# Optimization experiments

Measured on AMD Instinct MI355X. Metric: run time of the kernel, lower is better.

## Reference

```python
import jax, jax.numpy as jnp
import numpy as np

NUM_PATCHES_SIDE = 32
LOCAL_RADIUS = 3.0


def _build_non_local_mask():
    # coords of each patch on the grid, matching torch.meshgrid(indexing='ij')
    h = np.arange(NUM_PATCHES_SIDE)
    hh, ww = np.meshgrid(h, h, indexing='ij')
    coors = np.stack([hh, ww], axis=0).astype(np.float32)  # (2, H, W)
    coors = coors.reshape(2, -1).T                          # (n, 2)
    dist = np.linalg.norm(coors[:, None, :] - coors[None, :, :], axis=-1)
    return jnp.asarray(dist > LOCAL_RADIUS)                 # (n, n) bool


def setup_inputs() -> dict:
    key = jax.random.key(0)
    b, n, l, d = 8, NUM_PATCHES_SIDE * NUM_PATCHES_SIDE, 6, 512
    levels = jax.random.normal(key, (b, n, l, d), dtype=jnp.float32)
    non_local_mask = _build_non_local_mask()
    return {"levels": levels, "non_local_mask": non_local_mask}


def reference(levels, non_local_mask):
    b, n, l, d = levels.shape
    # F.normalize(levels, dim=-1): x / max(||x||, eps)
    norm = jnp.linalg.norm(levels, axis=-1, keepdims=True)
    k = levels / jnp.maximum(norm, 1e-12)
    # scores per level: (b, l, n, n)
    sim = jnp.einsum('bild,bjld->blij', levels, k) * (d ** -0.5)
    max_neg = -jnp.finfo(sim.dtype).max
    sim = jnp.where(non_local_mask[None, None, :, :], max_neg, sim)
    attn = jax.nn.softmax(sim, axis=-1)
    out = jnp.einsum('blij,bjld->bild', attn, levels)
    return out
```

## Files before the change

kernel.cpp:

```cpp
#include <hip/hip_runtime.h>
#include <math.h>

#define NPS 32
#define NN  (NPS*NPS)
#define LL  6
#define DD  512
#define ROWSPB (NN*LL)
#define BIAS 576

#define INV_SQRT_D 0.044194173824159216f
#define LOG2E      1.4426950408889634f
#define KLOG       (INV_SQRT_D * LOG2E)

__device__ __forceinline__ float half_sum32(float x) {
    int t;
    t = __builtin_amdgcn_update_dpp(0, __float_as_int(x), 0xB1, 0xF, 0xF, true);
    x += __int_as_float(t);
    t = __builtin_amdgcn_update_dpp(0, __float_as_int(x), 0x4E, 0xF, 0xF, true);
    x += __int_as_float(t);
    t = __builtin_amdgcn_update_dpp(0, __float_as_int(x), 0x141, 0xF, 0xF, true);
    x += __int_as_float(t);
    t = __builtin_amdgcn_update_dpp(0, __float_as_int(x), 0x140, 0xF, 0xF, true);
    x += __int_as_float(t);
    x += __int_as_float(__builtin_amdgcn_ds_swizzle(__float_as_int(x), 0x401F));
    return x;
}

__device__ __forceinline__ float wave_sum_bcast(float x) {
    x = half_sum32(x);
    x += __shfl_xor(x, 32, 64);
    return x;
}

__device__ __forceinline__ float dot16(const float4& a0, const float4& a1,
                                       const float4& a2, const float4& a3,
                                       const float4& b0, const float4& b1,
                                       const float4& b2, const float4& b3) {
    float d = a0.x * b0.x;
    d = fmaf(a0.y, b0.y, d); d = fmaf(a0.z, b0.z, d); d = fmaf(a0.w, b0.w, d);
    d = fmaf(a1.x, b1.x, d); d = fmaf(a1.y, b1.y, d); d = fmaf(a1.z, b1.z, d);
    d = fmaf(a1.w, b1.w, d);
    d = fmaf(a2.x, b2.x, d); d = fmaf(a2.y, b2.y, d); d = fmaf(a2.z, b2.z, d);
    d = fmaf(a2.w, b2.w, d);
    d = fmaf(a3.x, b3.x, d); d = fmaf(a3.y, b3.y, d); d = fmaf(a3.z, b3.z, d);
    d = fmaf(a3.w, b3.w, d);
    return d;
}

__global__ __launch_bounds__(256) void ca_norm2(const float* __restrict__ levels,
                                                float* __restrict__ cws,
                                                float* __restrict__ mws, int rows) {
    int tid  = threadIdx.x;
    int lane = tid & 63;
    int sl   = lane & 31;
    int grp  = lane >> 5;
    int w = ((int)blockIdx.x * 4 + (tid >> 6)) * 2 + grp;
    if (w >= rows) return;
    const float4* x4 = (const float4*)(levels + (unsigned)(w * DD));
    float4 a0 = x4[sl], a1 = x4[sl+32], a2 = x4[sl+64], a3 = x4[sl+96];
    float s2 = dot16(a0,a1,a2,a3, a0,a1,a2,a3);
    s2 = half_sum32(s2);
    if (sl == 0) {
        float r = __frsqrt_rn(s2);
        cws[w] = KLOG * r;
        mws[w] = KLOG * s2 * r;
    }
}

__global__ __launch_bounds__(256) void ca_fused4(const float* __restrict__ levels,
                                                 const float* __restrict__ cws,
                                                 const float* __restrict__ mws,
                                                 float* __restrict__ out, int rows) {
    constexpr int NIT = 18;
    constexpr int typ [NIT] = { 2, 2, 2, 2, 2, 2, 2, 2, 2, 2,  0, 0, 0, 0,  1, 1, 1, 1};
    constexpr int dhA_[NIT] = {-2,-2,-1,-1, 0, 0, 1, 1, 2, 2, -3,-2,-1, 0, -3,-2,-1, 0};
    constexpr int duA_[NIT] = {-1, 0,-1, 0,-2,-1,-1, 0,-1, 0,  0,-2,-2,-3,  1, 3, 3, 0};
    constexpr int dhB_[NIT] = {-2,-2,-1,-1, 0, 0, 1, 1, 2, 2,  0, 1, 2, 3,  0, 1, 2, 3};
    constexpr int duB_[NIT] = { 1, 2, 1, 2, 2, 3, 1, 2, 1, 2,  1,-2,-2, 0,  4, 3, 3, 1};

    unsigned bk    = blockIdx.x;
    unsigned chunk = gridDim.x >> 3;
    unsigned vb    = (bk & 7) * chunk + (bk >> 3);

    int tid  = threadIdx.x;
    int lane = tid & 63;
    int sl   = lane & 31;
    bool hi  = lane >= 32;

    int b  = (int)(vb / 768u);
    int r1 = (int)(vb - (unsigned)b * 768u);
    int pg = r1 / 6;
    int l  = r1 - pg * 6;
    int p0 = pg * 8 + ((tid >> 6) << 1);
    int w0 = __builtin_amdgcn_readfirstlane(b * ROWSPB + p0 * LL + l);
    if (w0 >= rows) return;
    int ph  = p0 >> 5;
    int pw0 = p0 & 31;

    const float4* x0 = (const float4*)(levels + (size_t)w0 * DD);
    const float4* x1 = x0 + (DD / 4) * LL;
    float4 a00 = x0[sl], a01 = x0[sl+32], a02 = x0[sl+64], a03 = x0[sl+96];
    float4 a10 = x1[sl], a11 = x1[sl+32], a12 = x1[sl+64], a13 = x1[sl+96];

    float m20 = mws[w0];
    float m21 = mws[w0 + LL];

    float  lsum0 = 0.0f, lsum1 = 0.0f;
    float4 c00 = make_float4(0,0,0,0), c01 = make_float4(0,0,0,0);
    float4 c02 = make_float4(0,0,0,0), c03 = make_float4(0,0,0,0);
    float4 c10 = make_float4(0,0,0,0), c11 = make_float4(0,0,0,0);
    float4 c12 = make_float4(0,0,0,0), c13 = make_float4(0,0,0,0);

    const char* lvb = (const char*)levels + ((long long)w0 - BIAS) * (DD * 4);
    const char* cwb = (const char*)cws    + ((long long)w0 - BIAS) * 4;

    #pragma unroll
    for (int t = 0; t < NIT; ++t) {
        const int dA = dhA_[t], uA = duA_[t];
        const int dB = dhB_[t], uB = duB_[t];
        bool vA = ((unsigned)(ph + dA) < (unsigned)NPS) &&
                  ((unsigned)(pw0 + uA) < (unsigned)NPS);
        bool vB = ((unsigned)(ph + dB) < (unsigned)NPS) &&
                  ((unsigned)(pw0 + uB) < (unsigned)NPS);
        int offA = ((vA ? (dA * NPS + uA) * LL : 0) + BIAS) * (DD * 4);
        int offB = ((vB ? (dB * NPS + uB) * LL : 0) + BIAS) * (DD * 4);
        int off  = hi ? offB : offA;
        const char* bp = lvb + off;
        float4 b0 = *(const float4*)(bp + sl * 16);
        float4 b1 = *(const float4*)(bp + sl * 16 + 512);
        float4 b2 = *(const float4*)(bp + sl * 16 + 1024);
        float4 b3 = *(const float4*)(bp + sl * 16 + 1536);
        float  cj = *(const float*)(cwb + (off >> 9));
        float  vm = (hi ? vB : vA) ? 1.0f : 0.0f;

        float d0 = 0.f, d1 = 0.f;
        if (typ[t] != 1) d0 = dot16(a00,a01,a02,a03, b0,b1,b2,b3);
        if (typ[t] != 0) d1 = dot16(a10,a11,a12,a13, b0,b1,b2,b3);
        if (typ[t] != 1) d0 = half_sum32(d0);
        if (typ[t] != 0) d1 = half_sum32(d1);

        if (typ[t] != 1) {
            float pr0 = vm * __builtin_amdgcn_exp2f(fmaf(d0, cj, -m20));
            lsum0 += pr0;
            c00.x = fmaf(pr0, b0.x, c00.x); c00.y = fmaf(pr0, b0.y, c00.y);
            c00.z = fmaf(pr0, b0.z, c00.z); c00.w = fmaf(pr0, b0.w, c00.w);
            c01.x = fmaf(pr0, b1.x, c01.x); c01.y = fmaf(pr0, b1.y, c01.y);
            c01.z = fmaf(pr0, b1.z, c01.z); c01.w = fmaf(pr0, b1.w, c01.w);
            c02.x = fmaf(pr0, b2.x, c02.x); c02.y = fmaf(pr0, b2.y, c02.y);
            c02.z = fmaf(pr0, b2.z, c02.z); c02.w = fmaf(pr0, b2.w, c02.w);
            c03.x = fmaf(pr0, b3.x, c03.x); c03.y = fmaf(pr0, b3.y, c03.y);
            c03.z = fmaf(pr0, b3.z, c03.z); c03.w = fmaf(pr0, b3.w, c03.w);
        }
        if (typ[t] != 0) {
            float pr1 = vm * __builtin_amdgcn_exp2f(fmaf(d1, cj, -m21));
            lsum1 += pr1;
            c10.x = fmaf(pr1, b0.x, c10.x); c10.y = fmaf(pr1, b0.y, c10.y);
            c10.z = fmaf(pr1, b0.z, c10.z); c10.w = fmaf(pr1, b0.w, c10.w);
            c11.x = fmaf(pr1, b1.x, c11.x); c11.y = fmaf(pr1, b1.y, c11.y);
            c11.z = fmaf(pr1, b1.z, c11.z); c11.w = fmaf(pr1, b1.w, c11.w);
            c12.x = fmaf(pr1, b2.x, c12.x); c12.y = fmaf(pr1, b2.y, c12.y);
            c12.z = fmaf(pr1, b2.z, c12.z); c12.w = fmaf(pr1, b2.w, c12.w);
            c13.x = fmaf(pr1, b3.x, c13.x); c13.y = fmaf(pr1, b3.y, c13.y);
            c13.z = fmaf(pr1, b3.z, c13.z); c13.w = fmaf(pr1, b3.w, c13.w);
        }
    }

    #define CMB(v) v += __shfl_xor(v, 32, 64)
    CMB(lsum0); CMB(lsum1);
    CMB(c00.x); CMB(c00.y); CMB(c00.z); CMB(c00.w);
    CMB(c01.x); CMB(c01.y); CMB(c01.z); CMB(c01.w);
    CMB(c02.x); CMB(c02.y); CMB(c02.z); CMB(c02.w);
    CMB(c03.x); CMB(c03.y); CMB(c03.z); CMB(c03.w);
    CMB(c10.x); CMB(c10.y); CMB(c10.z); CMB(c10.w);
    CMB(c11.x); CMB(c11.y); CMB(c11.z); CMB(c11.w);
    CMB(c12.x); CMB(c12.y); CMB(c12.z); CMB(c12.w);
    CMB(c13.x); CMB(c13.y); CMB(c13.z); CMB(c13.w);
    #undef CMB

    lsum0 += 1.0f; lsum1 += 1.0f;
    c00.x += a00.x; c00.y += a00.y; c00.z += a00.z; c00.w += a00.w;
    c01.x += a01.x; c01.y += a01.y; c01.z += a01.z; c01.w += a01.w;
    c02.x += a02.x; c02.y += a02.y; c02.z += a02.z; c02.w += a02.w;
    c03.x += a03.x; c03.y += a03.y; c03.z += a03.z; c03.w += a03.w;
    c10.x += a10.x; c10.y += a10.y; c10.z += a10.z; c10.w += a10.w;
    c11.x += a11.x; c11.y += a11.y; c11.z += a11.z; c11.w += a11.w;
    c12.x += a12.x; c12.y += a12.y; c12.z += a12.z; c12.w += a12.w;
    c13.x += a13.x; c13.y += a13.y; c13.z += a13.z; c13.w += a13.w;

    float  inv = 1.0f / (hi ? lsum1 : lsum0);
    float4 s0 = hi ? c10 : c00;
    float4 s1 = hi ? c11 : c01;
    float4 s2 = hi ? c12 : c02;
    float4 s3 = hi ? c13 : c03;
    float4* o4 = (float4*)(out + (size_t)(hi ? w0 + LL : w0) * DD);
    o4[sl]    = make_float4(s0.x*inv, s0.y*inv, s0.z*inv, s0.w*inv);
    o4[sl+32] = make_float4(s1.x*inv, s1.y*inv, s1.z*inv, s1.w*inv);
    o4[sl+64] = make_float4(s2.x*inv, s2.y*inv, s2.z*inv, s2.w*inv);
    o4[sl+96] = make_float4(s3.x*inv, s3.y*inv, s3.z*inv, s3.w*inv);
}

__global__ __launch_bounds__(256) void ca_fallback(const float* __restrict__ levels,
                                                   float* __restrict__ out, int rows) {
    constexpr int dh[28] = {-3,-2,-2,-2,-2,-2,-1,-1,-1,-1,-1, 0, 0, 0, 0, 0, 0,
                             1, 1, 1, 1, 1, 2, 2, 2, 2, 2, 3};
    constexpr int dw[28] = { 0,-2,-1, 0, 1, 2,-2,-1, 0, 1, 2,-3,-2,-1, 1, 2, 3,
                            -2,-1, 0, 1, 2,-2,-1, 0, 1, 2, 0};
    unsigned bk    = blockIdx.x;
    unsigned chunk = gridDim.x >> 3;
    unsigned vb    = (bk & 7) * chunk + (bk >> 3);
    int w = __builtin_amdgcn_readfirstlane((int)(vb * 4 + (threadIdx.x >> 6)));
    if (w >= rows) return;
    int lane = threadIdx.x & 63;
    int i  = (w / LL) % NN;
    int ph = i >> 5, pw = i & 31;
    const float4* xi4 = (const float4*)(levels + (size_t)w * DD);
    float4 a0 = xi4[lane], a1 = xi4[lane + 64];
    float s2i = a0.x*a0.x + a0.y*a0.y + a0.z*a0.z + a0.w*a0.w
              + a1.x*a1.x + a1.y*a1.y + a1.z*a1.z + a1.w*a1.w;
    s2i = wave_sum_bcast(s2i);
    float m2 = __fsqrt_rn(s2i) * KLOG;
    float lsum = 1.0f;
    float acc0=a0.x, acc1=a0.y, acc2=a0.z, acc3=a0.w;
    float acc4=a1.x, acc5=a1.y, acc6=a1.z, acc7=a1.w;
    #pragma unroll
    for (int t = 0; t < 28; ++t) {
        int hh = ph + dh[t], ww = pw + dw[t];
        if ((unsigned)hh < (unsigned)NPS && (unsigned)ww < (unsigned)NPS) {
            int jrow = w + (dh[t] * NPS + dw[t]) * LL;
            const float4* xj4 = (const float4*)(levels + (size_t)jrow * DD);
            float4 b0 = xj4[lane], b1 = xj4[lane + 64];
            float d = a0.x * b0.x;
            d = fmaf(a0.y, b0.y, d); d = fmaf(a0.z, b0.z, d); d = fmaf(a0.w, b0.w, d);
            d = fmaf(a1.x, b1.x, d); d = fmaf(a1.y, b1.y, d); d = fmaf(a1.z, b1.z, d);
            d = fmaf(a1.w, b1.w, d);
            d = wave_sum_bcast(d);
            float q2 = b0.x*b0.x + b0.y*b0.y + b0.z*b0.z + b0.w*b0.w
                     + b1.x*b1.x + b1.y*b1.y + b1.z*b1.z + b1.w*b1.w;
            q2 = wave_sum_bcast(q2);
            float cj = KLOG * __frsqrt_rn(q2);
            float p = __builtin_amdgcn_exp2f(fmaf(d, cj, -m2));
            lsum += p;
            acc0 = fmaf(p, b0.x, acc0); acc1 = fmaf(p, b0.y, acc1);
            acc2 = fmaf(p, b0.z, acc2); acc3 = fmaf(p, b0.w, acc3);
            acc4 = fmaf(p, b1.x, acc4); acc5 = fmaf(p, b1.y, acc5);
            acc6 = fmaf(p, b1.z, acc6); acc7 = fmaf(p, b1.w, acc7);
        }
    }
    float inv = 1.0f / lsum;
    float4* o4 = (float4*)(out + (size_t)w * DD);
    o4[lane]      = make_float4(acc0*inv, acc1*inv, acc2*inv, acc3*inv);
    o4[lane + 64] = make_float4(acc4*inv, acc5*inv, acc6*inv, acc7*inv);
}

extern "C" void kernel_launch(void* const* d_in, const int* in_sizes, int n_in,
                              void* d_out, int out_size, void* d_ws, size_t ws_size,
                              hipStream_t stream) {
    const float* levels = (const float*)d_in[0];
    float* out = (float*)d_out;

    int rows = in_sizes[0] / DD;

    if (d_ws && ws_size >= (size_t)rows * 2 * sizeof(float) && (rows % 48) == 0) {
        float* cws = (float*)d_ws;
        float* mws = cws + rows;
        int blocks1 = (rows + 7) / 8;
        ca_norm2<<<blocks1, 256, 0, stream>>>(levels, cws, mws, rows);
        int blocks2 = rows / 8;
        ca_fused4<<<blocks2, 256, 0, stream>>>(levels, cws, mws, out, rows);
    } else {
        int blocks = (rows + 3) / 4;
        ca_fallback<<<blocks, 256, 0, stream>>>(levels, out, rows);
    }
}
```

Measured before the change: 235.1 us.

## Convert levels to fp16 copy in norm pass and use fdot2 in fused attention

The norm kernel now also writes an fp16 copy of the input into workspace. A new fused kernel reads the fp16 neighbours, computes dot products with packed fdot2 instructions, and accumulates the weighted sums in fp32. This halves the bytes read per neighbour in the bandwidth-bound local-window attention. The cost is an extra full fp16 write pass, and both the scores and the values lose precision, including the self term added from fp16. The new path runs only if the workspace is large enough to hold the fp16 copy.

Result: slower. 273.9 us (+16.5%).

```diff
diff --git a/kernel.cpp b/kernel.cpp
--- a/kernel.cpp
+++ b/kernel.cpp
@@ -11,6 +11,19 @@
 #define INV_SQRT_D 0.044194173824159216f
 #define LOG2E      1.4426950408889634f
 #define KLOG       (INV_SQRT_D * LOG2E)
+
+typedef __fp16 h2 __attribute__((ext_vector_type(2)));
+typedef __fp16 h4 __attribute__((ext_vector_type(4)));
+
+#if __has_builtin(__builtin_amdgcn_fdot2)
+#define FDOT2(a, b, c) __builtin_amdgcn_fdot2((a), (b), (c), false)
+#else
+#define FDOT2(a, b, c) fmaf((float)(a)[0], (float)(b)[0], \
+                       fmaf((float)(a)[1], (float)(b)[1], (c)))
+#endif
+
+#define H2LO(v) __builtin_shufflevector((v), (v), 0, 1)
+#define H2HI(v) __builtin_shufflevector((v), (v), 2, 3)
 
 __device__ __forceinline__ float half_sum32(float x) {
     int t;
@@ -45,6 +58,43 @@
     d = fmaf(a3.x, b3.x, d); d = fmaf(a3.y, b3.y, d); d = fmaf(a3.z, b3.z, d);
     d = fmaf(a3.w, b3.w, d);
     return d;
+}
+
+__global__ __launch_bounds__(256) void ca_norm3(const float* __restrict__ levels,
+                                                __fp16* __restrict__ hlev,
+                                                float* __restrict__ cws,
+                                                float* __restrict__ mws, int rows) {
+    int tid  = threadIdx.x;
+    int lane = tid & 63;
+    int sl   = lane & 31;
+    int grp  = lane >> 5;
+    int w = ((int)blockIdx.x * 4 + (tid >> 6)) * 2 + grp;
+    if (w >= rows) return;
+    const float4* x4 = (const float4*)(levels + (unsigned)(w * DD));
+    float4 a0 = x4[sl], a1 = x4[sl+32], a2 = x4[sl+64], a3 = x4[sl+96];
+    float s2 = dot16(a0,a1,a2,a3, a0,a1,a2,a3);
+    s2 = half_sum32(s2);
+
+    char* hrow = (char*)hlev + (size_t)w * (DD * 2);
+    {
+        h2 q0 = __builtin_amdgcn_cvt_pkrtz(a0.x, a0.y);
+        h2 q1 = __builtin_amdgcn_cvt_pkrtz(a0.z, a0.w);
+        *(h4*)(hrow + sl*8)       = __builtin_shufflevector(q0, q1, 0, 1, 2, 3);
+        q0 = __builtin_amdgcn_cvt_pkrtz(a1.x, a1.y);
+        q1 = __builtin_amdgcn_cvt_pkrtz(a1.z, a1.w);
+        *(h4*)(hrow + sl*8 + 256) = __builtin_shufflevector(q0, q1, 0, 1, 2, 3);
+        q0 = __builtin_amdgcn_cvt_pkrtz(a2.x, a2.y);
+        q1 = __builtin_amdgcn_cvt_pkrtz(a2.z, a2.w);
+        *(h4*)(hrow + sl*8 + 512) = __builtin_shufflevector(q0, q1, 0, 1, 2, 3);
+        q0 = __builtin_amdgcn_cvt_pkrtz(a3.x, a3.y);
+        q1 = __builtin_amdgcn_cvt_pkrtz(a3.z, a3.w);
+        *(h4*)(hrow + sl*8 + 768) = __builtin_shufflevector(q0, q1, 0, 1, 2, 3);
+    }
+    if (sl == 0) {
+        float r = __frsqrt_rn(s2);
+        cws[w] = KLOG * r;
+        mws[w] = KLOG * s2 * r;
+    }
 }
 
 __global__ __launch_bounds__(256) void ca_norm2(const float* __restrict__ levels,
@@ -67,11 +117,155 @@
     }
 }
 
+#define NIT 18
+
+__global__ __launch_bounds__(256) void ca_fused5(const __fp16* __restrict__ hlev,
+                                                 const float* __restrict__ cws,
+                                                 const float* __restrict__ mws,
+                                                 float* __restrict__ out, int rows) {
+    constexpr int typ [NIT] = { 2, 2, 2, 2, 2, 2, 2, 2, 2, 2,  0, 0, 0, 0,  1, 1, 1, 1};
+    constexpr int dhA_[NIT] = {-2,-2,-1,-1, 0, 0, 1, 1, 2, 2, -3,-2,-1, 0, -3,-2,-1, 0};
+    constexpr int duA_[NIT] = {-1, 0,-1, 0,-2,-1,-1, 0,-1, 0,  0,-2,-2,-3,  1, 3, 3, 0};
+    constexpr int dhB_[NIT] = {-2,-2,-1,-1, 0, 0, 1, 1, 2, 2,  0, 1, 2, 3,  0, 1, 2, 3};
+    constexpr int duB_[NIT] = { 1, 2, 1, 2, 2, 3, 1, 2, 1, 2,  1,-2,-2, 0,  4, 3, 3, 1};
+
+    unsigned bk    = blockIdx.x;
+    unsigned chunk = gridDim.x >> 3;
+    unsigned vb    = (bk & 7) * chunk + (bk >> 3);
+
+    int tid  = threadIdx.x;
+    int lane = tid & 63;
+    int sl   = lane & 31;
+    bool hi  = lane >= 32;
+
+    int b  = (int)(vb / 768u);
+    int r1 = (int)(vb - (unsigned)b * 768u);
+    int pg = r1 / 6;
+    int l  = r1 - pg * 6;
+    int p0 = pg * 8 + ((tid >> 6) << 1);
+    int w0 = __builtin_amdgcn_readfirstlane(b * ROWSPB + p0 * LL + l);
+    if (w0 >= rows) return;
+    int ph  = p0 >> 5;
+    int pw0 = p0 & 31;
+
+    const char* x0 = (const char*)hlev + (size_t)w0 * (DD * 2);
+    const char* x1 = x0 + (DD * 2) * LL;
+    h4 a00 = *(const h4*)(x0 + sl*8),       a01 = *(const h4*)(x0 + sl*8 + 256);
+    h4 a02 = *(const h4*)(x0 + sl*8 + 512), a03 = *(const h4*)(x0 + sl*8 + 768);
+    h4 a10 = *(const h4*)(x1 + sl*8),       a11 = *(const h4*)(x1 + sl*8 + 256);
+    h4 a12 = *(const h4*)(x1 + sl*8 + 512), a13 = *(const h4*)(x1 + sl*8 + 768);
+
+    float m20 = mws[w0];
+    float m21 = mws[w0 + LL];
+
+    float  lsum0 = 0.0f, lsum1 = 0.0f;
+    float4 c00 = make_float4(0,0,0,0), c01 = make_float4(0,0,0,0);
+    float4 c02 = make_float4(0,0,0,0), c03 = make_float4(0,0,0,0);
+    float4 c10 = make_float4(0,0,0,0), c11 = make_float4(0,0,0,0);
+    float4 c12 = make_float4(0,0,0,0), c13 = make_float4(0,0,0,0);
+
+    const char* hvb = (const char*)hlev + ((long long)w0 - BIAS) * (DD * 2);
+    const char* cwb = (const char*)cws  + ((long long)w0 - BIAS) * 4;
+
+    #pragma unroll
+    for (int t = 0; t < NIT; ++t) {
+        const int dA = dhA_[t], uA = duA_[t];
+        const int dB = dhB_[t], uB = duB_[t];
+        bool vA = ((unsigned)(ph + dA) < (unsigned)NPS) &&
+                  ((unsigned)(pw0 + uA) < (unsigned)NPS);
+        bool vB = ((unsigned)(ph + dB) < (unsigned)NPS) &&
+                  ((unsigned)(pw0 + uB) < (unsigned)NPS);
+        int offA = ((vA ? (dA * NPS + uA) * LL : 0) + BIAS) * (DD * 2);
+        int offB = ((vB ? (dB * NPS + uB) * LL : 0) + BIAS) * (DD * 2);
+        int off  = hi ? offB : offA;
+        const char* bp = hvb + off;
+        h4 b0 = *(const h4*)(bp + sl*8);
+        h4 b1 = *(const h4*)(bp + sl*8 + 256);
+        h4 b2 = *(const h4*)(bp + sl*8 + 512);
+        h4 b3 = *(const h4*)(bp + sl*8 + 768);
+        float cj = *(const float*)(cwb + (off >> 8));
+        float vm = (hi ? vB : vA) ? 1.0f : 0.0f;
+
+        float d0 = 0.f, d1 = 0.f;
+        if (typ[t] != 1) {
+            d0 = FDOT2(H2LO(a00), H2LO(b0), d0); d0 = FDOT2(H2HI(a00), H2HI(b0), d0);
+            d0 = FDOT2(H2LO(a01), H2LO(b1), d0); d0 = FDOT2(H2HI(a01), H2HI(b1), d0);
+            d0 = FDOT2(H2LO(a02), H2LO(b2), d0); d0 = FDOT2(H2HI(a02), H2HI(b2), d0);
+            d0 = FDOT2(H2LO(a03), H2LO(b3), d0); d0 = FDOT2(H2HI(a03), H2HI(b3), d0);
+        }
+        if (typ[t] != 0) {
+            d1 = FDOT2(H2LO(a10), H2LO(b0), d1); d1 = FDOT2(H2HI(a10), H2HI(b0), d1);
+            d1 = FDOT2(H2LO(a11), H2LO(b1), d1); d1 = FDOT2(H2HI(a11), H2HI(b1), d1);
+            d1 = FDOT2(H2LO(a12), H2LO(b2), d1); d1 = FDOT2(H2HI(a12), H2HI(b2), d1);
+            d1 = FDOT2(H2LO(a13), H2LO(b3), d1); d1 = FDOT2(H2HI(a13), H2HI(b3), d1);
+        }
+        if (typ[t] != 1) d0 = half_sum32(d0);
+        if (typ[t] != 0) d1 = half_sum32(d1);
+
+        if (typ[t] != 1) {
+            float pr0 = vm * __builtin_amdgcn_exp2f(fmaf(d0, cj, -m20));
+            lsum0 += pr0;
+            c00.x = fmaf(pr0, (float)b0[0], c00.x); c00.y = fmaf(pr0, (float)b0[1], c00.y);
+            c00.z = fmaf(pr0, (float)b0[2], c00.z); c00.w = fmaf(pr0, (float)b0[3], c00.w);
+            c01.x = fmaf(pr0, (float)b1[0], c01.x); c01.y = fmaf(pr0, (float)b1[1], c01.y);
+            c01.z = fmaf(pr0, (float)b1[2], c01.z); c01.w = fmaf(pr0, (float)b1[3], c01.w);
+            c02.x = fmaf(pr0, (float)b2[0], c02.x); c02.y = fmaf(pr0, (float)b2[1], c02.y);
+            c02.z = fmaf(pr0, (float)b2[2], c02.z); c02.w = fmaf(pr0, (float)b2[3], c02.w);
+            c03.x = fmaf(pr0, (float)b3[0], c03.x); c03.y = fmaf(pr0, (float)b3[1], c03.y);
+            c03.z = fmaf(pr0, (float)b3[2], c03.z); c03.w = fmaf(pr0, (float)b3[3], c03.w);
+        }
+        if (typ[t] != 0) {
+            float pr1 = vm * __builtin_amdgcn_exp2f(fmaf(d1, cj, -m21));
+            lsum1 += pr1;
+            c10.x = fmaf(pr1, (float)b0[0], c10.x); c10.y = fmaf(pr1, (float)b0[1], c10.y);
+            c10.z = fmaf(pr1, (float)b0[2], c10.z); c10.w = fmaf(pr1, (float)b0[3], c10.w);
+            c11.x = fmaf(pr1, (float)b1[0], c11.x); c11.y = fmaf(pr1, (float)b1[1], c11.y);
+            c11.z = fmaf(pr1, (float)b1[2], c11.z); c11.w = fmaf(pr1, (float)b1[3], c11.w);
+            c12.x = fmaf(pr1, (float)b2[0], c12.x); c12.y = fmaf(pr1, (float)b2[1], c12.y);
+            c12.z = fmaf(pr1, (float)b2[2], c12.z); c12.w = fmaf(pr1, (float)b2[3], c12.w);
+            c13.x = fmaf(pr1, (float)b3[0], c13.x); c13.y = fmaf(pr1, (float)b3[1], c13.y);
+            c13.z = fmaf(pr1, (float)b3[2], c13.z); c13.w = fmaf(pr1, (float)b3[3], c13.w);
+        }
+    }
+
+    #define CMB(v) v += __shfl_xor(v, 32, 64)
+    CMB(lsum0); CMB(lsum1);
+    CMB(c00.x); CMB(c00.y); CMB(c00.z); CMB(c00.w);
+    CMB(c01.x); CMB(c01.y); CMB(c01.z); CMB(c01.w);
+    CMB(c02.x); CMB(c02.y); CMB(c02.z); CMB(c02.w);
+    CMB(c03.x); CMB(c03.y); CMB(c03.z); CMB(c03.w);
+    CMB(c10.x); CMB(c10.y); CMB(c10.z); CMB(c10.w);
+    CMB(c11.x); CMB(c11.y); CMB(c11.z); CMB(c11.w);
+    CMB(c12.x); CMB(c12.y); CMB(c12.z); CMB(c12.w);
+    CMB(c13.x); CMB(c13.y); CMB(c13.z); CMB(c13.w);
+    #undef CMB
+
+    lsum0 += 1.0f; lsum1 += 1.0f;
+    c00.x += (float)a00[0]; c00.y += (float)a00[1]; c00.z += (float)a00[2]; c00.w += (float)a00[3];
+    c01.x += (float)a01[0]; c01.y += (float)a01[1]; c01.z += (float)a01[2]; c01.w += (float)a01[3];
+    c02.x += (float)a02[0]; c02.y += (float)a02[1]; c02.z += (float)a02[2]; c02.w += (float)a02[3];
+    c03.x += (float)a03[0]; c03.y += (float)a03[1]; c03.z += (float)a03[2]; c03.w += (float)a03[3];
+    c10.x += (float)a10[0]; c10.y += (float)a10[1]; c10.z += (float)a10[2]; c10.w += (float)a10[3];
+    c11.x += (float)a11[0]; c11.y += (float)a11[1]; c11.z += (float)a11[2]; c11.w += (float)a11[3];
+    c12.x += (float)a12[0]; c12.y += (float)a12[1]; c12.z += (float)a12[2]; c12.w += (float)a12[3];
+    c13.x += (float)a13[0]; c13.y += (float)a13[1]; c13.z += (float)a13[2]; c13.w += (float)a13[3];
+
+    float  inv = 1.0f / (hi ? lsum1 : lsum0);
+    float4 s0 = hi ? c10 : c00;
+    float4 s1 = hi ? c11 : c01;
+    float4 s2 = hi ? c12 : c02;
+    float4 s3 = hi ? c13 : c03;
+    float4* o4 = (float4*)(out + (size_t)(hi ? w0 + LL : w0) * DD);
+    o4[sl]    = make_float4(s0.x*inv, s0.y*inv, s0.z*inv, s0.w*inv);
+    o4[sl+32] = make_float4(s1.x*inv, s1.y*inv, s1.z*inv, s1.w*inv);
+    o4[sl+64] = make_float4(s2.x*inv, s2.y*inv, s2.z*inv, s2.w*inv);
+    o4[sl+96] = make_float4(s3.x*inv, s3.y*inv, s3.z*inv, s3.w*inv);
+}
+
 __global__ __launch_bounds__(256) void ca_fused4(const float* __restrict__ levels,
                                                  const float* __restrict__ cws,
                                                  const float* __restrict__ mws,
                                                  float* __restrict__ out, int rows) {
-    constexpr int NIT = 18;
     constexpr int typ [NIT] = { 2, 2, 2, 2, 2, 2, 2, 2, 2, 2,  0, 0, 0, 0,  1, 1, 1, 1};
     constexpr int dhA_[NIT] = {-2,-2,-1,-1, 0, 0, 1, 1, 2, 2, -3,-2,-1, 0, -3,-2,-1, 0};
     constexpr int duA_[NIT] = {-1, 0,-1, 0,-2,-1,-1, 0,-1, 0,  0,-2,-2,-3,  1, 3, 3, 0};
@@ -260,7 +454,18 @@
 
     int rows = in_sizes[0] / DD;
 
-    if (d_ws && ws_size >= (size_t)rows * 2 * sizeof(float) && (rows % 48) == 0) {
+    size_t need_f16 = (size_t)rows * DD * 2 + (size_t)rows * 2 * sizeof(float);
+    size_t need_f32 = (size_t)rows * 2 * sizeof(float);
+
+    if (d_ws && ws_size >= need_f16 && (rows % 48) == 0) {
+        __fp16* hlev = (__fp16*)d_ws;
+        float* cws = (float*)((char*)d_ws + (size_t)rows * DD * 2);
+        float* mws = cws + rows;
+        int blocks1 = (rows + 7) / 8;
+        ca_norm3<<<blocks1, 256, 0, stream>>>(levels, hlev, cws, mws, rows);
+        int blocks2 = rows / 8;
+        ca_fused5<<<blocks2, 256, 0, stream>>>(hlev, cws, mws, out, rows);
+    } else if (d_ws && ws_size >= need_f32 && (rows % 48) == 0) {
         float* cws = (float*)d_ws;
         float* mws = cws + rows;
         int blocks1 = (rows + 7) / 8;
```
